# Optimization experiments

Measured on AMD Instinct MI355X. Metric: run time of the kernel, lower is better.

Reference implementation:

```python
import jax, jax.numpy as jnp
import numpy as np

EPS = 1e-6

def layer_norm(x, g, b):
    mu = jnp.mean(x, axis=-1, keepdims=True)
    var = jnp.mean((x - mu) ** 2, axis=-1, keepdims=True)
    return g * (x - mu) / jnp.sqrt(var + EPS) + b

def linear_mha(v_in, k_in, q_in, wq, bq, wk, bk, wv, bv, wo, bo, num_heads, d_model):
    b, s, _ = q_in.shape
    dv = d_model // num_heads
    q = q_in @ wq + bq                       # [b, s, h] (depth-1 per head)
    k = k_in @ wk + bk                       # [b, s, h]
    v = (v_in @ wv + bv).reshape(b, s, num_heads, dv).transpose(0, 2, 1, 3)  # [b,h,s,dv]
    q = q.transpose(0, 2, 1)                 # [b, h, s]
    k = k.transpose(0, 2, 1)                 # [b, h, s]
    # phi(k)^T v collapses seq: rank-1 per head -> [b, h, dv]
    kv = jnp.einsum('bhs,bhsd->bhd', jax.nn.sigmoid(k), v)
    # NOTE: tf.cumsum(axis=1) on shape (b, h, 1, dv) cumsums over the HEAD axis
    s_cum = jnp.cumsum(kv, axis=1)           # [b, h, dv]
    out = jnp.einsum('bhs,bhd->bhsd', jax.nn.sigmoid(q), s_cum)  # [b,h,s,dv]
    out = out.transpose(0, 2, 1, 3).reshape(b, s, d_model)
    return out @ wo + bo

def setup_inputs() -> dict:
    key = jax.random.key(0)
    ks = jax.random.split(key, 24)
    B, S, D, H, F = 4, 4096, 1024, 16, 4096
    gl = lambda k, shp: jax.random.uniform(k, shp, jnp.float32,
        -jnp.sqrt(6.0 / (shp[0] + shp[1])), jnp.sqrt(6.0 / (shp[0] + shp[1])))
    inp = {
        'x': jax.random.normal(ks[0], (B, S, D), jnp.float32),
        'enc': jax.random.normal(ks[1], (B, S, D), jnp.float32),
        'wq1': gl(ks[2], (D, H)), 'bq1': jnp.zeros((H,), jnp.float32),
        'wk1': gl(ks[3], (D, H)), 'bk1': jnp.zeros((H,), jnp.float32),
        'wv1': gl(ks[4], (D, D)), 'bv1': jnp.zeros((D,), jnp.float32),
        'wo1': gl(ks[5], (D, D)), 'bo1': jnp.zeros((D,), jnp.float32),
        'wq2': gl(ks[6], (D, H)), 'bq2': jnp.zeros((H,), jnp.float32),
        'wk2': gl(ks[7], (D, H)), 'bk2': jnp.zeros((H,), jnp.float32),
        'wv2': gl(ks[8], (D, D)), 'bv2': jnp.zeros((D,), jnp.float32),
        'wo2': gl(ks[9], (D, D)), 'bo2': jnp.zeros((D,), jnp.float32),
        'wf1': gl(ks[10], (D, F)), 'bf1': jnp.zeros((F,), jnp.float32),
        'wf2': gl(ks[11], (F, D)), 'bf2': jnp.zeros((D,), jnp.float32),
        'g1': jnp.ones((D,), jnp.float32), 'be1': jnp.zeros((D,), jnp.float32),
        'g2': jnp.ones((D,), jnp.float32), 'be2': jnp.zeros((D,), jnp.float32),
        'g3': jnp.ones((D,), jnp.float32), 'be3': jnp.zeros((D,), jnp.float32),
    }
    return inp

def reference(x, enc, wq1, bq1, wk1, bk1, wv1, bv1, wo1, bo1,
              wq2, bq2, wk2, bk2, wv2, bv2, wo2, bo2,
              wf1, bf1, wf2, bf2, g1, be1, g2, be2, g3, be3):
    H, D = 16, x.shape[-1]
    attn1 = linear_mha(x, x, x, wq1, bq1, wk1, bk1, wv1, bv1, wo1, bo1, H, D)
    out1 = layer_norm(attn1 + x, g1, be1)
    attn2 = linear_mha(enc, enc, out1, wq2, bq2, wk2, bk2, wv2, bv2, wo2, bo2, H, D)
    out2 = layer_norm(attn2 + out1, g2, be2)
    ffn = jax.nn.relu(out2 @ wf1 + bf1) @ wf2 + bf2
    out3 = layer_norm(ffn + out2, g3, be3)
    return (out3, jnp.zeros_like(out3), jnp.zeros_like(out3))
```

## Files before the change

### kernel.cpp

```cpp
#include <hip/hip_runtime.h>
#include <cstdint>

typedef unsigned short u16;
typedef __bf16 bf16x8 __attribute__((ext_vector_type(8)));
typedef float f32x4 __attribute__((ext_vector_type(4)));

__device__ __forceinline__ float bf2f(u16 h) {
  union { uint32_t u; float f; } v; v.u = (uint32_t)h << 16; return v.f;
}
__device__ __forceinline__ u16 f2bf(float f) {
  union { float f; uint32_t u; } v; v.f = f;
  uint32_t r = v.u + 0x7fffu + ((v.u >> 16) & 1u);
  return (u16)(r >> 16);
}
__device__ __forceinline__ float sigmoidf_(float x) {
  return 1.0f / (1.0f + __expf(-x));
}
__device__ __forceinline__ void load_lds16(const void* g, void* l) {
  __builtin_amdgcn_global_load_lds(
      (const __attribute__((address_space(1))) void*)g,
      (__attribute__((address_space(3))) void*)l, 16, 0, 0);
}
__device__ __forceinline__ bf16x8 cvt8(const float* p) {
  float4 a = *(const float4*)p, b = *(const float4*)(p + 4);
  union { u16 u[8]; bf16x8 v; } r;
  r.u[0] = f2bf(a.x); r.u[1] = f2bf(a.y); r.u[2] = f2bf(a.z); r.u[3] = f2bf(a.w);
  r.u[4] = f2bf(b.x); r.u[5] = f2bf(b.y); r.u[6] = f2bf(b.z); r.u[7] = f2bf(b.w);
  return r.v;
}
#define BAR() __builtin_amdgcn_s_barrier()

__global__ __launch_bounds__(256) void transpose_cvt(
    const float* __restrict__ in, u16* __restrict__ out, int K, int N) {
  __shared__ float t[32][33];
  int n0 = blockIdx.x * 32, k0 = blockIdx.y * 32;
  int tx = threadIdx.x & 31, ty = threadIdx.x >> 5;
#pragma unroll
  for (int i = 0; i < 32; i += 8)
    t[ty + i][tx] = in[(long)(k0 + ty + i) * N + n0 + tx];
  __syncthreads();
#pragma unroll
  for (int i = 0; i < 32; i += 8)
    out[(long)(n0 + ty + i) * K + k0 + tx] = f2bf(t[tx][ty + i]);
}

template <int SAME, int QBF>
__global__ __launch_bounds__(256) void proj_mfma(
    const void* __restrict__ xq_, const float* __restrict__ xk,
    const float* __restrict__ wq, const float* __restrict__ bq,
    const float* __restrict__ wk, const float* __restrict__ bk,
    float* __restrict__ qout, float* __restrict__ kout) {
  __shared__ __attribute__((aligned(16))) u16 wt[2][16384];
  const int tid = threadIdx.x;
  for (int kq = 0; kq < 4; kq++) {
    int k = kq * 256 + tid;
    const float4* q4 = (const float4*)(wq + (long)k * 16);
    const float4* k4 = (const float4*)(wk + (long)k * 16);
#pragma unroll
    for (int p = 0; p < 4; p++) {
      float4 qv = q4[p], kv = k4[p];
      float qf[4] = {qv.x, qv.y, qv.z, qv.w};
      float kf[4] = {kv.x, kv.y, kv.z, kv.w};
#pragma unroll
      for (int j = 0; j < 4; j++) {
        int c = p * 4 + j;
        int off = (c * 2048 + k * 2) ^ ((c & 7) << 4);
        *(u16*)((char*)wt[0] + off) = f2bf(qf[j]);
        *(u16*)((char*)wt[1] + off) = f2bf(kf[j]);
      }
    }
  }
  __syncthreads();
  const int wv = tid >> 6, lane = tid & 63;
  const int lrow = lane & 15, g = lane >> 4;
  const long tok0 = (long)blockIdx.x * 64 + wv * 16;
  const int swz = (lrow & 7) << 4;
  const long arow = (tok0 + lrow) * 1024 + g * 8;
  f32x4 accq = {}, acck = {};
#pragma unroll 8
  for (int ks = 0; ks < 32; ks++) {
    bf16x8 aq_;
    if (QBF)
      aq_ = *(const bf16x8*)((const u16*)xq_ + arow + ks * 32);
    else
      aq_ = cvt8((const float*)xq_ + arow + ks * 32);
    bf16x8 ak_;
    if (SAME)
      ak_ = aq_;
    else
      ak_ = cvt8(xk + arow + ks * 32);
    int off = (lrow * 2048 + ks * 64 + g * 16) ^ swz;
    bf16x8 bq_ = *(const bf16x8*)((const char*)wt[0] + off);
    bf16x8 bk_ = *(const bf16x8*)((const char*)wt[1] + off);
    accq = __builtin_amdgcn_mfma_f32_16x16x32_bf16(aq_, bq_, accq, 0, 0, 0);
    acck = __builtin_amdgcn_mfma_f32_16x16x32_bf16(ak_, bk_, acck, 0, 0, 0);
  }
  const int col = lrow, r0 = g * 4;
  float bqv = bq[col], bkv = bk[col];
#pragma unroll
  for (int i = 0; i < 4; i++) {
    qout[(tok0 + r0 + i) * 16 + col] = accq[i] + bqv;
    kout[(tok0 + r0 + i) * 16 + col] = acck[i] + bkv;
  }
}

__global__ __launch_bounds__(256) void ksum(const float* __restrict__ kp,
                                            const float* __restrict__ x,
                                            float* __restrict__ ypart,
                                            float* __restrict__ spart) {
  __shared__ __attribute__((aligned(16))) float sk[256][20];
  __shared__ float ssl[16][17];
  const int tid = threadIdx.x;
  const int cc = blockIdx.x, sc = blockIdx.y, b = blockIdx.z;
  const int cl = tid & 63, sg = tid >> 6;
  const int col0 = cc * 128 + cl;
  float acc0[16], acc1[16];
#pragma unroll
  for (int h = 0; h < 16; h++) { acc0[h] = 0.f; acc1[h] = 0.f; }
  float ss = 0.f;
  for (int tile = 0; tile < 2; tile++) {
    const int s0 = sc * 512 + tile * 256;
    const float* kr = kp + ((long)b * 4096 + s0 + tid) * 16;
#pragma unroll
    for (int p = 0; p < 4; p++) {
      float4 k4 = *(const float4*)(kr + p * 4);
      *(float4*)&sk[tid][p * 4] = make_float4(
          sigmoidf_(k4.x), sigmoidf_(k4.y), sigmoidf_(k4.z), sigmoidf_(k4.w));
    }
    __syncthreads();
    {
      int g2 = tid >> 4, h2 = tid & 15;
      float s_ = 0.f;
#pragma unroll
      for (int i = 0; i < 16; i++) s_ += sk[g2 * 16 + i][h2];
      ssl[g2][h2] = s_;
    }
    __syncthreads();
    if (tid < 16) {
      float s_ = 0.f;
#pragma unroll
      for (int gg = 0; gg < 16; gg++) s_ += ssl[gg][tid];
      ss += s_;
    }
    const float* xr = x + ((long)b * 4096 + s0 + sg * 64) * 1024 + col0;
    for (int j = 0; j < 64; j++) {
      float xv0 = xr[(long)j * 1024];
      float xv1 = xr[(long)j * 1024 + 64];
      const float4* skr = (const float4*)sk[sg * 64 + j];
#pragma unroll
      for (int p = 0; p < 4; p++) {
        float4 s4 = skr[p];
        acc0[p * 4 + 0] += s4.x * xv0; acc1[p * 4 + 0] += s4.x * xv1;
        acc0[p * 4 + 1] += s4.y * xv0; acc1[p * 4 + 1] += s4.y * xv1;
        acc0[p * 4 + 2] += s4.z * xv0; acc1[p * 4 + 2] += s4.z * xv1;
        acc0[p * 4 + 3] += s4.w * xv0; acc1[p * 4 + 3] += s4.w * xv1;
      }
    }
    __syncthreads();
  }
  long pbase = (long)(b * 32 + sc * 4 + sg) * 16384 + col0;
#pragma unroll
  for (int h = 0; h < 16; h++) {
    ypart[pbase + h * 1024] = acc0[h];
    ypart[pbase + h * 1024 + 64] = acc1[h];
  }
  if (tid < 16) spart[(b * 8 + sc) * 16 + tid] = ss;
}

__global__ __launch_bounds__(256) void kv_small(
    const float* __restrict__ ypart, const float* __restrict__ spart,
    const float* __restrict__ wvw, const float* __restrict__ bv,
    float* __restrict__ kv) {
  __shared__ float yl[1024];
  __shared__ float red[4][64];
  const int tid = threadIdx.x;
  const int b = blockIdx.x >> 4, h = blockIdx.x & 15;
  for (int c = tid; c < 1024; c += 256) {
    float s_ = 0.f;
    const float* yp = ypart + (long)(b * 32) * 16384 + h * 1024 + c;
#pragma unroll
    for (int p = 0; p < 32; p++) s_ += yp[(long)p * 16384];
    yl[c] = s_;
  }
  __syncthreads();
  const int wv_ = tid >> 6, d = tid & 63;
  float acc = 0.f;
  const float* wcol = wvw + h * 64 + d;
  for (int c = wv_ * 256; c < wv_ * 256 + 256; c++)
    acc += yl[c] * wcol[(long)c * 1024];
  red[wv_][d] = acc;
  __syncthreads();
  if (tid < 64) {
    float ss = 0.f;
#pragma unroll
    for (int s_ = 0; s_ < 8; s_++) ss += spart[(b * 8 + s_) * 16 + h];
    kv[(b * 16 + h) * 64 + tid] = red[0][tid] + red[1][tid] + red[2][tid] +
                                  red[3][tid] + ss * bv[h * 64 + tid];
  }
}

__global__ __launch_bounds__(256) void zker(const float* __restrict__ kvb,
                                            const float* __restrict__ wo,
                                            float* __restrict__ z) {
  __shared__ float sc_[64];
  const int tid = threadIdx.x;
  const int b = blockIdx.x >> 4, h = blockIdx.x & 15;
  if (tid < 64) {
    float run = 0.f;
    for (int hh = 0; hh <= h; hh++) run += kvb[(b * 16 + hh) * 64 + tid];
    sc_[tid] = run;
  }
  __syncthreads();
  float4 acc = make_float4(0.f, 0.f, 0.f, 0.f);
  for (int d = 0; d < 64; d++) {
    float s_ = sc_[d];
    float4 w = ((const float4*)(wo + (long)(h * 64 + d) * 1024))[tid];
    acc.x += s_ * w.x; acc.y += s_ * w.y;
    acc.z += s_ * w.z; acc.w += s_ * w.w;
  }
  ((float4*)(z + (long)(b * 16 + h) * 1024))[tid] = acc;
}

template <int OMODE>
__global__ __launch_bounds__(256) void ln_attn(
    const float* __restrict__ qp, const float* __restrict__ z,
    const float* __restrict__ bo, const float* __restrict__ r,
    const float* __restrict__ g, const float* __restrict__ be,
    float* __restrict__ outf, u16* __restrict__ outb) {
  __shared__ float zs[16][1024];
  __shared__ float sq16[16];
  __shared__ float s1[4], s2[4];
  const int tid = threadIdx.x;
  const int b = blockIdx.x >> 8;
  const float4* zg = (const float4*)(z + (long)b * 16384);
  float4* zl = (float4*)zs;
#pragma unroll
  for (int i = 0; i < 16; i++) zl[i * 256 + tid] = zg[i * 256 + tid];
  float4 gv = ((const float4*)g)[tid];
  float4 bev = ((const float4*)be)[tid];
  float4 bov = ((const float4*)bo)[tid];
  const int wid = tid >> 6, lane = tid & 63;
  for (int rr_ = 0; rr_ < 16; rr_++) {
    long row = (long)blockIdx.x * 16 + rr_;
    if (tid < 16) sq16[tid] = sigmoidf_(qp[row * 16 + tid]);
    __syncthreads();
    float4 rv = ((const float4*)(r + row * 1024))[tid];
    float y0 = bov.x + rv.x, y1 = bov.y + rv.y;
    float y2 = bov.z + rv.z, y3 = bov.w + rv.w;
#pragma unroll
    for (int h = 0; h < 16; h++) {
      float s_ = sq16[h];
      float4 zv = *(const float4*)&zs[h][tid * 4];
      y0 += s_ * zv.x; y1 += s_ * zv.y; y2 += s_ * zv.z; y3 += s_ * zv.w;
    }
    float s = y0 + y1 + y2 + y3;
    float q = y0 * y0 + y1 * y1 + y2 * y2 + y3 * y3;
#pragma unroll
    for (int o = 32; o > 0; o >>= 1) {
      s += __shfl_down(s, o);
      q += __shfl_down(q, o);
    }
    if (lane == 0) { s1[wid] = s; s2[wid] = q; }
    __syncthreads();
    s = s1[0] + s1[1] + s1[2] + s1[3];
    q = s2[0] + s2[1] + s2[2] + s2[3];
    float mu = s * (1.f / 1024.f);
    float var = q * (1.f / 1024.f) - mu * mu;
    float inv = rsqrtf(fmaxf(var, 0.f) + 1e-6f);
    float o0 = gv.x * (y0 - mu) * inv + bev.x;
    float o1 = gv.y * (y1 - mu) * inv + bev.y;
    float o2 = gv.z * (y2 - mu) * inv + bev.z;
    float o3 = gv.w * (y3 - mu) * inv + bev.w;
    ((float4*)(outf + row * 1024))[tid] = make_float4(o0, o1, o2, o3);
    if (OMODE == 2) {
      uint2 ob;
      ob.x = (uint32_t)f2bf(o0) | ((uint32_t)f2bf(o1) << 16);
      ob.y = (uint32_t)f2bf(o2) | ((uint32_t)f2bf(o3) << 16);
      ((uint2*)(outb + row * 1024))[tid] = ob;
    }
    __syncthreads();
  }
}

template <int ACT>
__global__ __launch_bounds__(512) void gemm256(
    const u16* __restrict__ A, const u16* __restrict__ BT,
    const float* __restrict__ bias, u16* __restrict__ C, int M, int N,
    int K) {
  __shared__ __attribute__((aligned(16))) u16 lds[65536];
  const int tid = threadIdx.x;
  const int wid = tid >> 6, lane = tid & 63;
  const int wm = wid >> 2, wn = wid & 3;
  const int lrow = lane & 15, g = lane >> 4;

  int nwg = gridDim.x * gridDim.y;
  int orig = blockIdx.y * gridDim.x + blockIdx.x;
  int wg = (nwg & 7) ? orig : ((orig & 7) * (nwg >> 3) + (orig >> 3));
  const long bn = (long)(wg % gridDim.x) * 256;
  const long bm = (long)(wg / gridDim.x) * 256;

  const int rr = wid * 16 + (lane >> 2);
  const int esrc = (((lane & 3) ^ ((lane >> 3) & 3)) * 8);
  const u16* Abase = A + (bm + rr) * (long)K + esrc;
  const u16* Bbase = BT + (bn + rr) * (long)K + esrc;
  const long jstep = (long)128 * K;
  char* ldsc = (char*)lds;
  const int ldsw = wid * 1024;

  const int slotr = (g ^ ((lrow >> 1) & 3)) * 16;
  const int aoff = (wm * 128 + lrow) * 64 + slotr;
  const int boff = 32768 + (wn * 64 + lrow) * 64 + slotr;

  f32x4 acc[8][4] = {};
  const int KT = K >> 6;

  auto stage2 = [&](int buf, int kk, int kt, int half) {
    int dA = buf * 65536 + kk * 16384 + ldsw;
    if (half == 0) {
      const u16* sA = Abase + (long)kt * 64 + kk * 32;
      load_lds16(sA, ldsc + dA);
      load_lds16(sA + jstep, ldsc + dA + 8192);
    } else {
      const u16* sB = Bbase + (long)kt * 64 + kk * 32;
      load_lds16(sB, ldsc + dA + 32768);
      load_lds16(sB + jstep, ldsc + dA + 40960);
    }
  };

#define LDAB8(BUF, KK)                                                      \
  {                                                                         \
    const char* _b = ldsc + (BUF) * 65536 + (KK) * 16384;                   \
    _Pragma("unroll") for (int m = 0; m < 4; m++)                           \
        af[m] = *(const bf16x8*)(_b + aoff + m * 1024);                     \
    _Pragma("unroll") for (int n = 0; n < 4; n++)                           \
        bq[n] = *(const bf16x8*)(_b + boff + n * 1024);                     \
  }
#define LDA4(BUF, KK)                                                       \
  {                                                                         \
    const char* _b = ldsc + (BUF) * 65536 + (KK) * 16384;                   \
    _Pragma("unroll") for (int m = 4; m < 8; m++)                           \
        af[m] = *(const bf16x8*)(_b + aoff + m * 1024);                     \
  }
#define MMA16(M0)                                                           \
  __builtin_amdgcn_s_setprio(1);                                            \
  _Pragma("unroll") for (int m = M0; m < M0 + 4; m++)                       \
  _Pragma("unroll") for (int n = 0; n < 4; n++)                             \
      acc[m][n] = __builtin_amdgcn_mfma_f32_16x16x32_bf16(af[m], bq[n],     \
                                                          acc[m][n], 0, 0,  \
                                                          0);               \
  __builtin_amdgcn_s_setprio(0);
#define WLG0() asm volatile("s_waitcnt lgkmcnt(0)" ::: "memory")
#define WVM4() asm volatile("s_waitcnt vmcnt(4)" ::: "memory")
#define WVM0() asm volatile("s_waitcnt vmcnt(0)" ::: "memory")

  bf16x8 af[8], bq[4];

  stage2(0, 0, 0, 0);
  stage2(0, 0, 0, 1);
  stage2(0, 1, 0, 0);
  stage2(0, 1, 0, 1);
  WVM4();
  BAR();

  for (int kt = 0; kt + 1 < KT; ++kt) {
    const int b0 = kt & 1, b1 = b0 ^ 1;
    LDAB8(b0, 0);
    stage2(b1, 0, kt + 1, 0);
    BAR(); WLG0();
    MMA16(0);
    BAR();
    LDA4(b0, 0);
    stage2(b1, 0, kt + 1, 1);
    WVM4();
    BAR(); WLG0();
    MMA16(4);
    BAR();
    LDAB8(b0, 1);
    stage2(b1, 1, kt + 1, 0);
    BAR(); WLG0();
    MMA16(0);
    BAR();
    LDA4(b0, 1);
    stage2(b1, 1, kt + 1, 1);
    WVM4();
    BAR(); WLG0();
    MMA16(4);
    BAR();
  }
  {
    const int b0 = (KT - 1) & 1;
    LDAB8(b0, 0);
    BAR(); WLG0();
    MMA16(0);
    BAR();
    LDA4(b0, 0);
    WVM0();
    BAR(); WLG0();
    MMA16(4);
    BAR();
    LDAB8(b0, 1);
    BAR(); WLG0();
    MMA16(0);
    BAR();
    LDA4(b0, 1);
    BAR(); WLG0();
    MMA16(4);
    BAR();
  }

#pragma unroll
  for (int n = 0; n < 4; n++) {
    int cl = wn * 64 + n * 16 + lrow;
    float bb = bias[bn + cl];
#pragma unroll
    for (int m = 0; m < 8; m++) {
      int rl = wm * 128 + m * 16 + g * 4;
#pragma unroll
      for (int i = 0; i < 4; i++) {
        float v = acc[m][n][i] + bb;
        if (ACT == 1) v = fmaxf(v, 0.f);
        lds[(rl + i) * 256 + cl] = f2bf(v);
      }
    }
  }
  BAR();
  const uint4* lv = (const uint4*)lds;
#pragma unroll
  for (int it = 0; it < 16; it++) {
    int idx = it * 512 + tid;
    int row = idx >> 5;
    int cu = (idx & 31) * 8;
    *(uint4*)&C[(bm + row) * (long)N + bn + cu] = lv[idx];
  }
#undef LDAB8
#undef LDA4
#undef MMA16
#undef WLG0
#undef WVM4
#undef WVM0
}

__global__ __launch_bounds__(256) void ln_res(const u16* __restrict__ a,
                                              const float* __restrict__ r,
                                              const float* __restrict__ g,
                                              const float* __restrict__ be,
                                              float* __restrict__ outf) {
  long row = blockIdx.x;
  int tid = threadIdx.x;
  uint2 av = ((const uint2*)(a + row * 1024))[tid];
  float4 rv = ((const float4*)(r + row * 1024))[tid];
  float y[4];
  y[0] = bf2f((u16)(av.x & 0xffff)) + rv.x;
  y[1] = bf2f((u16)(av.x >> 16)) + rv.y;
  y[2] = bf2f((u16)(av.y & 0xffff)) + rv.z;
  y[3] = bf2f((u16)(av.y >> 16)) + rv.w;
  float s = y[0] + y[1] + y[2] + y[3];
  float q = y[0] * y[0] + y[1] * y[1] + y[2] * y[2] + y[3] * y[3];
#pragma unroll
  for (int o = 32; o > 0; o >>= 1) {
    s += __shfl_down(s, o);
    q += __shfl_down(q, o);
  }
  __shared__ float s1[4], s2[4];
  int wid = tid >> 6, lane = tid & 63;
  if (lane == 0) { s1[wid] = s; s2[wid] = q; }
  __syncthreads();
  s = s1[0] + s1[1] + s1[2] + s1[3];
  q = s2[0] + s2[1] + s2[2] + s2[3];
  float mu = s * (1.f / 1024.f);
  float var = q * (1.f / 1024.f) - mu * mu;
  float inv = rsqrtf(fmaxf(var, 0.f) + 1e-6f);
  float4 gv = ((const float4*)g)[tid], bv = ((const float4*)be)[tid];
  float o0 = gv.x * (y[0] - mu) * inv + bv.x;
  float o1 = gv.y * (y[1] - mu) * inv + bv.y;
  float o2 = gv.z * (y[2] - mu) * inv + bv.z;
  float o3 = gv.w * (y[3] - mu) * inv + bv.w;
  ((float4*)(outf + row * 1024))[tid] = make_float4(o0, o1, o2, o3);
}

extern "C" void kernel_launch(void* const* d_in, const int* in_sizes, int n_in,
                              void* d_out, int out_size, void* d_ws,
                              size_t ws_size, hipStream_t stream) {
  const float* x   = (const float*)d_in[0];
  const float* enc = (const float*)d_in[1];
  const float* wq1 = (const float*)d_in[2];  const float* bq1 = (const float*)d_in[3];
  const float* wk1 = (const float*)d_in[4];  const float* bk1 = (const float*)d_in[5];
  const float* wv1 = (const float*)d_in[6];  const float* bv1 = (const float*)d_in[7];
  const float* wo1 = (const float*)d_in[8];  const float* bo1 = (const float*)d_in[9];
  const float* wq2 = (const float*)d_in[10]; const float* bq2 = (const float*)d_in[11];
  const float* wk2 = (const float*)d_in[12]; const float* bk2 = (const float*)d_in[13];
  const float* wv2 = (const float*)d_in[14]; const float* bv2 = (const float*)d_in[15];
  const float* wo2 = (const float*)d_in[16]; const float* bo2 = (const float*)d_in[17];
  const float* wf1 = (const float*)d_in[18]; const float* bf1 = (const float*)d_in[19];
  const float* wf2 = (const float*)d_in[20]; const float* bf2 = (const float*)d_in[21];
  const float* g1 = (const float*)d_in[22];  const float* be1 = (const float*)d_in[23];
  const float* g2 = (const float*)d_in[24];  const float* be2 = (const float*)d_in[25];
  const float* g3 = (const float*)d_in[26];  const float* be3 = (const float*)d_in[27];
  (void)in_sizes; (void)n_in; (void)out_size; (void)ws_size;

  const size_t S = (size_t)16384 * 1024;
  float* O0 = (float*)d_out;

  char* base = (char*)d_ws;
  size_t off = 0;
  auto alloc = [&](size_t bytes) -> void* {
    void* p = base + off;
    off += (bytes + 255) & ~(size_t)255;
    return p;
  };
  u16* WT1    = (u16*)alloc((size_t)4096 * 1024 * 2);
  u16* WT2    = (u16*)alloc((size_t)4096 * 1024 * 2);
  float* qb   = (float*)alloc((size_t)16384 * 16 * 4);
  float* kb   = (float*)alloc((size_t)16384 * 16 * 4);
  float* ypart= (float*)alloc((size_t)4 * 32 * 16 * 1024 * 4);
  float* spart= (float*)alloc((size_t)4 * 8 * 16 * 4);
  float* kvb  = (float*)alloc((size_t)4 * 16 * 64 * 4);
  float* zb   = (float*)alloc((size_t)4 * 16 * 1024 * 4);
  u16* FA     = (u16*)alloc(S * 2);
  u16* FM     = (u16*)alloc((size_t)16384 * 4096 * 2);
  u16* O2b    = (u16*)alloc(S * 2);
  float* O1f  = (float*)alloc(S * 4);
  float* O2f  = (float*)alloc(S * 4);

  const int T = 16384;
  dim3 blk(256), gblk(512);

  proj_mfma<1, 0><<<256, blk, 0, stream>>>(x, nullptr, wq1, bq1, wk1, bk1,
                                           qb, kb);
  ksum<<<dim3(8, 8, 4), blk, 0, stream>>>(kb, x, ypart, spart);
  kv_small<<<64, blk, 0, stream>>>(ypart, spart, wv1, bv1, kvb);
  zker<<<64, blk, 0, stream>>>(kvb, wo1, zb);
  ln_attn<1><<<1024, blk, 0, stream>>>(qb, zb, bo1, x, g1, be1, O1f, nullptr);

  proj_mfma<0, 0><<<256, blk, 0, stream>>>(O1f, enc, wq2, bq2, wk2, bk2,
                                           qb, kb);
  ksum<<<dim3(8, 8, 4), blk, 0, stream>>>(kb, enc, ypart, spart);
  kv_small<<<64, blk, 0, stream>>>(ypart, spart, wv2, bv2, kvb);
  zker<<<64, blk, 0, stream>>>(kvb, wo2, zb);
  ln_attn<2><<<1024, blk, 0, stream>>>(qb, zb, bo2, O1f, g2, be2, O2f, O2b);

  transpose_cvt<<<dim3(128, 32), blk, 0, stream>>>(wf1, WT1, 1024, 4096);
  transpose_cvt<<<dim3(32, 128), blk, 0, stream>>>(wf2, WT2, 4096, 1024);
  gemm256<1><<<dim3(16, 64), gblk, 0, stream>>>(O2b, WT1, bf1, FM, T, 4096, 1024);
  gemm256<0><<<dim3(4, 64), gblk, 0, stream>>>(FM, WT2, bf2, FA, T, 1024, 4096);
  ln_res<<<16384, blk, 0, stream>>>(FA, O2f, g3, be3, O0);

  hipMemsetAsync((float*)d_out + S, 0, 2 * S * 4, stream);
}
```

Baseline: 589.5 us.

## Shrink FFN GEMM tile to 256x128 with smaller LDS for higher occupancy

Rewrites the FFN GEMM kernel from a 256x256 tile with K-step 64 and a 128 KB LDS double buffer into a 256x128 tile with K-step 32 and a 48 KB double buffer. Per-wave accumulators drop from 8x4 to 4x4, and launch_bounds asks for multiple workgroups per CU, so more blocks can be resident and hide latency. The pipeline is simplified to one barrier per K-step, and the epilogue writes the output in two halves through the reduced LDS. In exchange, arithmetic intensity per tile falls, more global loads are issued, and the full vmcnt(0) wait each step exposes more memory latency.

```diff
diff --git a/kernel.cpp b/kernel.cpp
--- a/kernel.cpp
+++ b/kernel.cpp
@@ -283,20 +283,20 @@
 }
 
 template <int ACT>
-__global__ __launch_bounds__(512) void gemm256(
+__global__ __launch_bounds__(512, 4) void gemm256(
     const u16* __restrict__ A, const u16* __restrict__ BT,
     const float* __restrict__ bias, u16* __restrict__ C, int M, int N,
     int K) {
-  __shared__ __attribute__((aligned(16))) u16 lds[65536];
+  __shared__ __attribute__((aligned(16))) u16 lds[24576];
   const int tid = threadIdx.x;
   const int wid = tid >> 6, lane = tid & 63;
-  const int wm = wid >> 2, wn = wid & 3;
+  const int wm = wid >> 1, wn = wid & 1;
   const int lrow = lane & 15, g = lane >> 4;
 
   int nwg = gridDim.x * gridDim.y;
   int orig = blockIdx.y * gridDim.x + blockIdx.x;
   int wg = (nwg & 7) ? orig : ((orig & 7) * (nwg >> 3) + (orig >> 3));
-  const long bn = (long)(wg % gridDim.x) * 256;
+  const long bn = (long)(wg % gridDim.x) * 128;
   const long bm = (long)(wg / gridDim.x) * 256;
 
   const int rr = wid * 16 + (lane >> 2);
@@ -308,135 +308,95 @@
   const int ldsw = wid * 1024;
 
   const int slotr = (g ^ ((lrow >> 1) & 3)) * 16;
-  const int aoff = (wm * 128 + lrow) * 64 + slotr;
-  const int boff = 32768 + (wn * 64 + lrow) * 64 + slotr;
-
-  f32x4 acc[8][4] = {};
-  const int KT = K >> 6;
-
-  auto stage2 = [&](int buf, int kk, int kt, int half) {
-    int dA = buf * 65536 + kk * 16384 + ldsw;
-    if (half == 0) {
-      const u16* sA = Abase + (long)kt * 64 + kk * 32;
-      load_lds16(sA, ldsc + dA);
-      load_lds16(sA + jstep, ldsc + dA + 8192);
-    } else {
-      const u16* sB = Bbase + (long)kt * 64 + kk * 32;
-      load_lds16(sB, ldsc + dA + 32768);
-      load_lds16(sB + jstep, ldsc + dA + 40960);
-    }
+  const int aoff0 = (wm * 64 + lrow) * 64 + slotr;
+  const int boff0 = 16384 + (wn * 64 + lrow) * 64 + slotr;
+
+  f32x4 acc[4][4] = {};
+  const int KT = K >> 5;
+
+  auto stage = [&](int s, int kt) {
+    const u16* sA = Abase + (long)kt * 32;
+    const u16* sB = Bbase + (long)kt * 32;
+    int d = s * 24576 + ldsw;
+    load_lds16(sA, ldsc + d);
+    load_lds16(sA + jstep, ldsc + d + 8192);
+    load_lds16(sB, ldsc + d + 16384);
   };
 
-#define LDAB8(BUF, KK)                                                      \
+#define LDAB(S)                                                             \
   {                                                                         \
-    const char* _b = ldsc + (BUF) * 65536 + (KK) * 16384;                   \
+    const char* _b = ldsc + (S) * 24576;                                    \
     _Pragma("unroll") for (int m = 0; m < 4; m++)                           \
-        af[m] = *(const bf16x8*)(_b + aoff + m * 1024);                     \
+        af[m] = *(const bf16x8*)(_b + aoff0 + m * 1024);                    \
     _Pragma("unroll") for (int n = 0; n < 4; n++)                           \
-        bq[n] = *(const bf16x8*)(_b + boff + n * 1024);                     \
-  }
-#define LDA4(BUF, KK)                                                       \
-  {                                                                         \
-    const char* _b = ldsc + (BUF) * 65536 + (KK) * 16384;                   \
-    _Pragma("unroll") for (int m = 4; m < 8; m++)                           \
-        af[m] = *(const bf16x8*)(_b + aoff + m * 1024);                     \
-  }
-#define MMA16(M0)                                                           \
+        bq[n] = *(const bf16x8*)(_b + boff0 + n * 1024);                    \
+  }
+#define MMA16()                                                             \
   __builtin_amdgcn_s_setprio(1);                                            \
-  _Pragma("unroll") for (int m = M0; m < M0 + 4; m++)                       \
+  _Pragma("unroll") for (int m = 0; m < 4; m++)                             \
   _Pragma("unroll") for (int n = 0; n < 4; n++)                             \
       acc[m][n] = __builtin_amdgcn_mfma_f32_16x16x32_bf16(af[m], bq[n],     \
                                                           acc[m][n], 0, 0,  \
                                                           0);               \
   __builtin_amdgcn_s_setprio(0);
 #define WLG0() asm volatile("s_waitcnt lgkmcnt(0)" ::: "memory")
-#define WVM4() asm volatile("s_waitcnt vmcnt(4)" ::: "memory")
 #define WVM0() asm volatile("s_waitcnt vmcnt(0)" ::: "memory")
 
-  bf16x8 af[8], bq[4];
-
-  stage2(0, 0, 0, 0);
-  stage2(0, 0, 0, 1);
-  stage2(0, 1, 0, 0);
-  stage2(0, 1, 0, 1);
-  WVM4();
+  bf16x8 af[4], bq[4];
+
+  stage(0, 0);
+  WVM0();
   BAR();
 
   for (int kt = 0; kt + 1 < KT; ++kt) {
-    const int b0 = kt & 1, b1 = b0 ^ 1;
-    LDAB8(b0, 0);
-    stage2(b1, 0, kt + 1, 0);
-    BAR(); WLG0();
-    MMA16(0);
+    const int s = kt & 1;
+    LDAB(s);
+    stage(s ^ 1, kt + 1);
+    WLG0();
+    MMA16();
+    WVM0();
     BAR();
-    LDA4(b0, 0);
-    stage2(b1, 0, kt + 1, 1);
-    WVM4();
-    BAR(); WLG0();
-    MMA16(4);
+  }
+  {
+    LDAB((KT - 1) & 1);
+    WLG0();
+    MMA16();
     BAR();
-    LDAB8(b0, 1);
-    stage2(b1, 1, kt + 1, 0);
-    BAR(); WLG0();
-    MMA16(0);
+  }
+
+  const uint4* lv = (const uint4*)lds;
+#pragma unroll
+  for (int half = 0; half < 2; half++) {
     BAR();
-    LDA4(b0, 1);
-    stage2(b1, 1, kt + 1, 1);
-    WVM4();
-    BAR(); WLG0();
-    MMA16(4);
+    if ((wm >> 1) == half) {
+#pragma unroll
+      for (int n = 0; n < 4; n++) {
+        int cl = wn * 64 + n * 16 + lrow;
+        float bb = bias[bn + cl];
+#pragma unroll
+        for (int m = 0; m < 4; m++) {
+          int rl = (wm & 1) * 64 + m * 16 + g * 4;
+#pragma unroll
+          for (int i = 0; i < 4; i++) {
+            float v = acc[m][n][i] + bb;
+            if (ACT == 1) v = fmaxf(v, 0.f);
+            lds[(rl + i) * 128 + cl] = f2bf(v);
+          }
+        }
+      }
+    }
     BAR();
-  }
-  {
-    const int b0 = (KT - 1) & 1;
-    LDAB8(b0, 0);
-    BAR(); WLG0();
-    MMA16(0);
-    BAR();
-    LDA4(b0, 0);
-    WVM0();
-    BAR(); WLG0();
-    MMA16(4);
-    BAR();
-    LDAB8(b0, 1);
-    BAR(); WLG0();
-    MMA16(0);
-    BAR();
-    LDA4(b0, 1);
-    BAR(); WLG0();
-    MMA16(4);
-    BAR();
-  }
-
-#pragma unroll
-  for (int n = 0; n < 4; n++) {
-    int cl = wn * 64 + n * 16 + lrow;
-    float bb = bias[bn + cl];
-#pragma unroll
-    for (int m = 0; m < 8; m++) {
-      int rl = wm * 128 + m * 16 + g * 4;
-#pragma unroll
-      for (int i = 0; i < 4; i++) {
-        float v = acc[m][n][i] + bb;
-        if (ACT == 1) v = fmaxf(v, 0.f);
-        lds[(rl + i) * 256 + cl] = f2bf(v);
-      }
-    }
-  }
-  BAR();
-  const uint4* lv = (const uint4*)lds;
-#pragma unroll
-  for (int it = 0; it < 16; it++) {
-    int idx = it * 512 + tid;
-    int row = idx >> 5;
-    int cu = (idx & 31) * 8;
-    *(uint4*)&C[(bm + row) * (long)N + bn + cu] = lv[idx];
-  }
-#undef LDAB8
-#undef LDA4
+#pragma unroll
+    for (int it = 0; it < 4; it++) {
+      int idx = it * 512 + tid;
+      int row = idx >> 4;
+      int cu = (idx & 15) * 8;
+      *(uint4*)&C[(bm + half * 128 + row) * (long)N + bn + cu] = lv[idx];
+    }
+  }
+#undef LDAB
 #undef MMA16
 #undef WLG0
-#undef WVM4
 #undef WVM0
 }
 
@@ -541,8 +501,8 @@
 
   transpose_cvt<<<dim3(128, 32), blk, 0, stream>>>(wf1, WT1, 1024, 4096);
   transpose_cvt<<<dim3(32, 128), blk, 0, stream>>>(wf2, WT2, 4096, 1024);
-  gemm256<1><<<dim3(16, 64), gblk, 0, stream>>>(O2b, WT1, bf1, FM, T, 4096, 1024);
-  gemm256<0><<<dim3(4, 64), gblk, 0, stream>>>(FM, WT2, bf2, FA, T, 1024, 4096);
+  gemm256<1><<<dim3(32, 64), gblk, 0, stream>>>(O2b, WT1, bf1, FM, T, 4096, 1024);
+  gemm256<0><<<dim3(8, 64), gblk, 0, stream>>>(FM, WT2, bf2, FA, T, 1024, 4096);
   ln_res<<<16384, blk, 0, stream>>>(FA, O2f, g3, be3, O0);
 
   hipMemsetAsync((float*)d_out + S, 0, 2 * S * 4, stream);
```

New measurement: 613.7 us. 1.04x slower.
